# Optimization experiments

Hardware: AMD Instinct MI355X
Metric: run time of the kernel (lower is better)

## Reference

```python
import jax, jax.numpy as jnp
import numpy as np


def setup_inputs() -> dict:
    key = jax.random.key(0)
    k1, k2 = jax.random.split(key)
    N, C, H, W = 8, 3, 512, 1024
    img = jax.random.normal(k1, (N, C, H, W), dtype=jnp.float32)
    flo = jax.random.normal(k2, (N, 2, H, W), dtype=jnp.float32)
    return {"img": img, "flo": flo}


def _splat(img_nhwc, ix, iy, w, H, W):
    # img_nhwc: (N,H,W,C); ix,iy: int32 (N,H,W) absolute target coords; w: (N,H,W)
    N = img_nhwc.shape[0]
    C = img_nhwc.shape[-1]
    valid = (ix >= 0) & (ix < H) & (iy >= 0) & (iy < W)
    w = jnp.where(valid, w, 0.0)
    ixc = jnp.clip(ix, 0, H - 1)
    iyc = jnp.clip(iy, 0, W - 1)
    n_idx = jnp.arange(N, dtype=jnp.int32)[:, None, None]
    tid = (n_idx * H + ixc) * W + iyc            # (N,H,W) flat index into N*H*W
    tid = tid.reshape(-1)
    vals = (img_nhwc * w[..., None]).reshape(-1, C)
    imgw = jnp.zeros((N * H * W, C), dtype=img_nhwc.dtype).at[tid].add(vals)
    onew = jnp.zeros((N * H * W,), dtype=img_nhwc.dtype).at[tid].add(w.reshape(-1))
    imgw = imgw.reshape(N, H, W, C).transpose(0, 3, 1, 2)          # (N,C,H,W)
    onew = jnp.broadcast_to(onew.reshape(N, 1, H, W), (N, C, H, W))
    return imgw, onew


def _forward(img, flo):
    N, C, H, W = img.shape
    y = flo[:, 0]                                # (N,H,W) row offset
    x = flo[:, 1]                                # (N,H,W) col offset
    x1 = jnp.floor(x); x2 = x1 + 1.0
    y1 = jnp.floor(y); y2 = y1 + 1.0
    # gaussian splat weights
    dx1 = (x - x1) ** 2; dx2 = (x - x2) ** 2
    dy1 = (y - y1) ** 2; dy2 = (y - y2) ** 2
    w11 = jnp.exp(-(dx1 + dy1)); w12 = jnp.exp(-(dx1 + dy2))
    w21 = jnp.exp(-(dx2 + dy1)); w22 = jnp.exp(-(dx2 + dy2))
    # base grid + integer shift -> absolute target coords
    bx = jnp.arange(H, dtype=jnp.int32)[None, :, None]   # row index
    by = jnp.arange(W, dtype=jnp.int32)[None, None, :]   # col index
    img_nhwc = img.transpose(0, 2, 3, 1)
    out = []
    for sx, sy, w in ((x1, y1, w11), (x1, y2, w12), (x2, y1, w21), (x2, y2, w22)):
        ix = sx.astype(jnp.int32) + bx
        iy = sy.astype(jnp.int32) + by
        out.append(_splat(img_nhwc, ix, iy, w, H, W))
    imgw = out[0][0] + out[1][0] + out[2][0] + out[3][0]
    o = out[0][1] + out[1][1] + out[2][1] + out[3][1]
    return imgw, o


def reference(img, flo):
    return _forward(img, flo)
```

## Files before the change

kernel.cpp:

```cpp
#include <hip/hip_runtime.h>
#include <stdint.h>

constexpr int Nn = 8;
constexpr int Cc = 3;
constexpr int Hh = 512;
constexpr int Ww = 1024;
constexpr int HW = Hh * Ww;
constexpr int NCHW = Nn * Cc * HW;

constexpr int TH = 16;
constexpr int TW = 32;
constexpr int R  = 4;
constexpr int RH = TH + 2 * R;
constexpr int RW = TW + 2 * R;
constexpr int NPIX = RH * RW;
constexpr int ITERS = (NPIX + 255) / 256;
constexpr int TILE_PIX = TH * TW;
constexpr int AWP = TW + 1;
constexpr int NP  = (TH + 1) * AWP;
constexpr int OVF_SLOTS = 3;

typedef float fvec4 __attribute__((ext_vector_type(4)));
typedef __attribute__((address_space(3))) float lds_f;

__device__ __forceinline__ void ds_fadd4(lds_f* p, float a, float b, float c, float d) {
    asm volatile(
        "ds_add_f32 %0, %1\n\t"
        "ds_add_f32 %0, %2 offset:2048\n\t"
        "ds_add_f32 %0, %3 offset:4096\n\t"
        "ds_add_f32 %0, %4 offset:6144"
        :: "v"(p), "v"(a), "v"(b), "v"(c), "v"(d) : "memory");
}

__global__ __launch_bounds__(256, 3) void splat_tiled(
        const float* __restrict__ img,
        const float* __restrict__ flo,
        float* __restrict__ out) {
    __shared__ unsigned int s_tag[NP];
    __shared__ unsigned int s_ocnt[(NP + 3) / 4];
    __shared__ alignas(16) float s_pay[NP * 4];
    __shared__ alignas(16) float s_ovf[OVF_SLOTS * NP * 4];
    __shared__ float s_pl[4 * TILE_PIX];
    const int tid = threadIdx.x;
    for (int i = tid; i < NP; i += 256) s_tag[i] = 0u;
    for (int i = tid; i < (NP + 3) / 4; i += 256) s_ocnt[i] = 0u;
    {
        fvec4* a4 = (fvec4*)s_pl;
        fvec4 z = {0.f, 0.f, 0.f, 0.f};
        a4[tid] = z;
        a4[tid + 256] = z;
    }
    __syncthreads();

    const int lin = blockIdx.x + 32 * blockIdx.y + 1024 * blockIdx.z;
    const int n   = lin & 7;
    const int t   = lin >> 3;
    const int tw0 = (t & 31) * TW;
    const int th0 = (t >> 5) * TH;
    const float* __restrict__ floy = flo + (size_t)(n * 2 + 0) * HW;
    const float* __restrict__ flox = flo + (size_t)(n * 2 + 1) * HW;
    const float* __restrict__ imgn = img + (size_t)n * Cc * HW;

    float sy[ITERS], sx[ITERS], u0[ITERS], u1[ITERS], u2[ITERS];
    #pragma unroll
    for (int it = 0; it < ITERS; ++it) {
        int i  = tid + 256 * it;
        int ic = i < NPIX ? i : NPIX - 1;
        int rh = ic / RW;
        int rw = ic - rh * RW;
        int h  = th0 - R + rh;
        int w  = tw0 - R + rw;
        int hc = h < 0 ? 0 : (h > Hh - 1 ? Hh - 1 : h);
        int wc = w < 0 ? 0 : (w > Ww - 1 ? Ww - 1 : w);
        int hwc = hc * Ww + wc;
        sy[it] = floy[hwc];
        sx[it] = flox[hwc];
        u0[it] = imgn[hwc];
        u1[it] = imgn[HW + hwc];
        u2[it] = imgn[2 * HW + hwc];
    }

    int aA[ITERS];
    unsigned int tg[ITERS], fxy[ITERS];
    #pragma unroll
    for (int it = 0; it < ITERS; ++it) {
        int i  = tid + 256 * it;
        int rh = i / RW;
        int rw = i - rh * RW;
        int h  = th0 - R + rh;
        int w  = tw0 - R + rw;
        bool live = (i < NPIX) & (h >= 0) & (h < Hh) & (w >= 0) & (w < Ww);

        float y = sy[it], x = sx[it];
        float x1f = floorf(x), y1f = floorf(y);
        float fx = x - x1f, fy = y - y1f;
        int ox = (int)x1f, oy = (int)y1f;
        bool patchok = (ox >= -R) & (ox <= R - 1) & (oy >= -R) & (oy <= R - 1);
        int ah = ox + rh - R;
        int aw = oy + rw - R;
        bool rec = live & patchok & (ah >= -1) & (ah <= TH - 1)
                                  & (aw >= -1) & (aw <= TW - 1);
        int aIdx = (ah + 1) * AWP + (aw + 1);
        tg[it]  = 0x80000000u | ((unsigned)(ox + 4) << 24) | ((unsigned)(oy + 4) << 16);
        fxy[it] = (unsigned)(fx * 65535.0f + 0.5f)
                | ((unsigned)(fy * 65535.0f + 0.5f) << 16);
        aA[it]  = rec ? aIdx : -1;
        if (rec) s_tag[aIdx] = tg[it];
    }
    __syncthreads();

    #pragma unroll
    for (int it = 0; it < ITERS; ++it) {
        int a = aA[it];
        if (a >= 0) {
            if (s_tag[a] == tg[it]) {
                fvec4 e = {u0[it], u1[it], u2[it], __uint_as_float(fxy[it])};
                *(fvec4*)&s_pay[a * 4] = e;
            } else {
                unsigned sh  = 8u * (unsigned)(a & 3);
                unsigned old = atomicAdd(&s_ocnt[a >> 2], 1u << sh);
                unsigned idx = (old >> sh) & 0xFFu;
                if (idx < (unsigned)OVF_SLOTS) {
                    fvec4 e = {u0[it], u1[it], u2[it], __uint_as_float(fxy[it])};
                    *(fvec4*)&s_ovf[((int)idx * NP + a) * 4] = e;
                } else {
                    int ah = a / AWP - 1;
                    int aw = a - (ah + 1) * AWP - 1;
                    float fx = (float)(fxy[it] & 0xFFFFu) * (1.0f / 65535.0f);
                    float fy = (float)(fxy[it] >> 16) * (1.0f / 65535.0f);
                    #pragma unroll
                    for (int ca = 0; ca < 2; ++ca) {
                        #pragma unroll
                        for (int cb = 0; cb < 2; ++cb) {
                            int t_h = ah + ca, t_w = aw + cb;
                            if ((unsigned)t_h < (unsigned)TH && (unsigned)t_w < (unsigned)TW) {
                                float dx = fx - (float)ca, dy = fy - (float)cb;
                                float wt = __expf(-(dx * dx + dy * dy));
                                ds_fadd4((lds_f*)s_pl + (t_h * TW + t_w),
                                         u0[it] * wt, u1[it] * wt, u2[it] * wt, wt);
                            }
                        }
                    }
                }
            }
        }
    }
    __syncthreads();

    float* __restrict__ imgw  = out;
    float* __restrict__ o_out = out + NCHW;
    const size_t nb = (size_t)n * Cc * HW;
    const fvec4* pay4 = (const fvec4*)s_pay;
    const fvec4* ovf4 = (const fvec4*)s_ovf;
    #pragma unroll
    for (int itr = 0; itr < 2; ++itr) {
        int pix = tid + 256 * itr;
        int lh = pix >> 5, lw = pix & 31;
        float s0 = s_pl[pix];
        float s1 = s_pl[TILE_PIX + pix];
        float s2 = s_pl[2 * TILE_PIX + pix];
        float s3 = s_pl[3 * TILE_PIX + pix];
        #pragma unroll
        for (int a = 0; a < 2; ++a) {
            #pragma unroll
            for (int b = 0; b < 2; ++b) {
                int ai = (lh - a + 1) * AWP + (lw - b + 1);
                unsigned tgv = s_tag[ai];
                if (tgv & 0x80000000u) {
                    fvec4 e = pay4[ai];
                    unsigned p = __float_as_uint(e[3]);
                    float fx = (float)(p & 0xFFFFu) * (1.0f / 65535.0f);
                    float fy = (float)(p >> 16) * (1.0f / 65535.0f);
                    float dx = fx - (float)a, dy = fy - (float)b;
                    float wt = __expf(-(dx * dx + dy * dy));
                    s0 += e[0] * wt; s1 += e[1] * wt; s2 += e[2] * wt; s3 += wt;
                }
                unsigned k = (s_ocnt[ai >> 2] >> (8u * (unsigned)(ai & 3))) & 0xFFu;
                #pragma unroll
                for (int j = 0; j < OVF_SLOTS; ++j) {
                    if (j < (int)k) {
                        fvec4 e = ovf4[j * NP + ai];
                        unsigned p = __float_as_uint(e[3]);
                        float fx = (float)(p & 0xFFFFu) * (1.0f / 65535.0f);
                        float fy = (float)(p >> 16) * (1.0f / 65535.0f);
                        float dx = fx - (float)a, dy = fy - (float)b;
                        float wt = __expf(-(dx * dx + dy * dy));
                        s0 += e[0] * wt; s1 += e[1] * wt; s2 += e[2] * wt; s3 += wt;
                    }
                }
            }
        }
        size_t hw = (size_t)(th0 + lh) * Ww + (tw0 + lw);
        __builtin_nontemporal_store(s0, imgw + nb + hw);
        __builtin_nontemporal_store(s1, imgw + nb + HW + hw);
        __builtin_nontemporal_store(s2, imgw + nb + 2 * HW + hw);
        __builtin_nontemporal_store(s3, o_out + nb + hw);
        __builtin_nontemporal_store(s3, o_out + nb + HW + hw);
        __builtin_nontemporal_store(s3, o_out + nb + 2 * HW + hw);
    }
}

__global__ __launch_bounds__(256) void rescan_all(
        const float* __restrict__ img,
        const float* __restrict__ flo,
        float* __restrict__ out) {
    float* imgw  = out;
    float* o_out = out + NCHW;
    unsigned int j = blockIdx.x * blockDim.x + threadIdx.x;
    if (j >= (unsigned)(Nn * HW / 4)) return;
    int n   = j / (HW / 4);
    int q   = j - n * (HW / 4);
    int hw0 = q * 4;
    const fvec4 y4 = *(const fvec4*)&flo[(size_t)(n * 2 + 0) * HW + hw0];
    const fvec4 x4 = *(const fvec4*)&flo[(size_t)(n * 2 + 1) * HW + hw0];
    #pragma unroll
    for (int k = 0; k < 4; ++k) {
        float x = x4[k], y = y4[k];
        if (x >= -(float)R && x < (float)R && y >= -(float)R && y < (float)R) continue;
        int hw = hw0 + k;
        int h = hw >> 10;
        int w = hw & (Ww - 1);
        float x1f = floorf(x), y1f = floorf(y);
        float fx = x - x1f, fy = y - y1f;
        int bx = (int)x1f, by = (int)y1f;
        float i0 = img[(size_t)(n * Cc + 0) * HW + hw];
        float i1 = img[(size_t)(n * Cc + 1) * HW + hw];
        float i2 = img[(size_t)(n * Cc + 2) * HW + hw];
        const size_t nb = (size_t)n * Cc * HW;
        #pragma unroll
        for (int a = 0; a < 2; ++a) {
            #pragma unroll
            for (int b = 0; b < 2; ++b) {
                int ix = h + bx + a;
                int iy = w + by + b;
                if (ix < 0 || ix >= Hh || iy < 0 || iy >= Ww) continue;
                float dx = fx - (float)a, dy = fy - (float)b;
                float wt = __expf(-(dx * dx + dy * dy));
                int t = ix * Ww + iy;
                atomicAdd(&imgw[nb + t], i0 * wt);
                atomicAdd(&imgw[nb + HW + t], i1 * wt);
                atomicAdd(&imgw[nb + 2 * HW + t], i2 * wt);
                atomicAdd(&o_out[nb + t], wt);
                atomicAdd(&o_out[nb + HW + t], wt);
                atomicAdd(&o_out[nb + 2 * HW + t], wt);
            }
        }
    }
}

extern "C" void kernel_launch(void* const* d_in, const int* in_sizes, int n_in,
                              void* d_out, int out_size, void* d_ws, size_t ws_size,
                              hipStream_t stream) {
    const float* img = (const float*)d_in[0];
    const float* flo = (const float*)d_in[1];
    float* out = (float*)d_out;
    (void)d_ws; (void)ws_size;

    dim3 block(256);
    dim3 grid(32, 32, 8);
    splat_tiled<<<grid, block, 0, stream>>>(img, flo, out);
    rescan_all<<<(Nn * HW / 4 + 255) / 256, 256, 0, stream>>>(img, flo, out);
}
```

Baseline: 209.0 us.

## Compress splat payload to fp16 slots and resolve collisions in rounds

```diff
diff --git a/kernel.cpp b/kernel.cpp
--- a/kernel.cpp
+++ b/kernel.cpp
@@ -1,4 +1,5 @@
 #include <hip/hip_runtime.h>
+#include <hip/hip_fp16.h>
 #include <stdint.h>
 
 constexpr int Nn = 8;
@@ -18,9 +19,10 @@
 constexpr int TILE_PIX = TH * TW;
 constexpr int AWP = TW + 1;
 constexpr int NP  = (TH + 1) * AWP;
-constexpr int OVF_SLOTS = 3;
+constexpr int NSLOT = 3;
 
 typedef float fvec4 __attribute__((ext_vector_type(4)));
+typedef float fvec2 __attribute__((ext_vector_type(2)));
 typedef __attribute__((address_space(3))) float lds_f;
 
 __device__ __forceinline__ void ds_fadd4(lds_f* p, float a, float b, float c, float d) {
@@ -32,18 +34,17 @@
         :: "v"(p), "v"(a), "v"(b), "v"(c), "v"(d) : "memory");
 }
 
-__global__ __launch_bounds__(256, 3) void splat_tiled(
+__global__ __launch_bounds__(256, 5) void splat_tiled(
         const float* __restrict__ img,
         const float* __restrict__ flo,
         float* __restrict__ out) {
     __shared__ unsigned int s_tag[NP];
-    __shared__ unsigned int s_ocnt[(NP + 3) / 4];
-    __shared__ alignas(16) float s_pay[NP * 4];
-    __shared__ alignas(16) float s_ovf[OVF_SLOTS * NP * 4];
+    __shared__ unsigned int s_pay[NSLOT * NP * 3];
+    __shared__ unsigned int s_kcnt[(NP + 3) / 4 + 1];
     __shared__ float s_pl[4 * TILE_PIX];
     const int tid = threadIdx.x;
     for (int i = tid; i < NP; i += 256) s_tag[i] = 0u;
-    for (int i = tid; i < (NP + 3) / 4; i += 256) s_ocnt[i] = 0u;
+    for (int i = tid; i < (NP + 3) / 4 + 1; i += 256) s_kcnt[i] = 0u;
     {
         fvec4* a4 = (fvec4*)s_pl;
         fvec4 z = {0.f, 0.f, 0.f, 0.f};
@@ -81,7 +82,8 @@
     }
 
     int aA[ITERS];
-    unsigned int tg[ITERS], fxy[ITERS];
+    unsigned int tg[ITERS], q0[ITERS], q1[ITERS], q2[ITERS];
+    bool pend[ITERS];
     #pragma unroll
     for (int it = 0; it < ITERS; ++it) {
         int i  = tid + 256 * it;
@@ -101,102 +103,127 @@
         bool rec = live & patchok & (ah >= -1) & (ah <= TH - 1)
                                   & (aw >= -1) & (aw <= TW - 1);
         int aIdx = (ah + 1) * AWP + (aw + 1);
-        tg[it]  = 0x80000000u | ((unsigned)(ox + 4) << 24) | ((unsigned)(oy + 4) << 16);
-        fxy[it] = (unsigned)(fx * 65535.0f + 0.5f)
-                | ((unsigned)(fy * 65535.0f + 0.5f) << 16);
-        aA[it]  = rec ? aIdx : -1;
+        tg[it] = 0x80000000u | ((unsigned)(ox + R) << 3) | (unsigned)(oy + R);
+        unsigned h0 = __half_as_ushort(__float2half_rn(u0[it]));
+        unsigned h1 = __half_as_ushort(__float2half_rn(u1[it]));
+        unsigned h2 = __half_as_ushort(__float2half_rn(u2[it]));
+        unsigned fxq = (unsigned)(fx * 65535.0f + 0.5f);
+        unsigned fyq = (unsigned)(fy * 65535.0f + 0.5f);
+        q0[it] = h0 | (h1 << 16);
+        q1[it] = h2 | (fxq << 16);
+        q2[it] = fyq;
+        aA[it]  = aIdx;
+        pend[it] = rec;
         if (rec) s_tag[aIdx] = tg[it];
     }
     __syncthreads();
 
     #pragma unroll
-    for (int it = 0; it < ITERS; ++it) {
-        int a = aA[it];
-        if (a >= 0) {
-            if (s_tag[a] == tg[it]) {
-                fvec4 e = {u0[it], u1[it], u2[it], __uint_as_float(fxy[it])};
-                *(fvec4*)&s_pay[a * 4] = e;
-            } else {
-                unsigned sh  = 8u * (unsigned)(a & 3);
-                unsigned old = atomicAdd(&s_ocnt[a >> 2], 1u << sh);
-                unsigned idx = (old >> sh) & 0xFFu;
-                if (idx < (unsigned)OVF_SLOTS) {
-                    fvec4 e = {u0[it], u1[it], u2[it], __uint_as_float(fxy[it])};
-                    *(fvec4*)&s_ovf[((int)idx * NP + a) * 4] = e;
-                } else {
-                    int ah = a / AWP - 1;
-                    int aw = a - (ah + 1) * AWP - 1;
-                    float fx = (float)(fxy[it] & 0xFFFFu) * (1.0f / 65535.0f);
-                    float fy = (float)(fxy[it] >> 16) * (1.0f / 65535.0f);
+    for (int r = 0; r < NSLOT; ++r) {
+        #pragma unroll
+        for (int it = 0; it < ITERS; ++it) {
+            if (pend[it] && s_tag[aA[it]] == tg[it]) {
+                int base = aA[it] * 9 + r * 3;
+                s_pay[base]     = q0[it];
+                s_pay[base + 1] = q1[it];
+                s_pay[base + 2] = q2[it];
+                ((unsigned char*)s_kcnt)[aA[it]] = (unsigned char)(r + 1);
+                pend[it] = false;
+            } else if (r == NSLOT - 1 && pend[it]) {
+                int a = aA[it];
+                int arow = a / AWP;
+                int ah = arow - 1;
+                int aw = a - arow * AWP - 1;
+                float fx = (float)(q1[it] >> 16) * (1.0f / 65535.0f);
+                float fy = (float)(q2[it] & 0xFFFFu) * (1.0f / 65535.0f);
+                float i0 = __half2float(__ushort_as_half((unsigned short)(q0[it] & 0xFFFFu)));
+                float i1 = __half2float(__ushort_as_half((unsigned short)(q0[it] >> 16)));
+                float i2 = __half2float(__ushort_as_half((unsigned short)(q1[it] & 0xFFFFu)));
+                #pragma unroll
+                for (int ca = 0; ca < 2; ++ca) {
                     #pragma unroll
-                    for (int ca = 0; ca < 2; ++ca) {
-                        #pragma unroll
-                        for (int cb = 0; cb < 2; ++cb) {
-                            int t_h = ah + ca, t_w = aw + cb;
-                            if ((unsigned)t_h < (unsigned)TH && (unsigned)t_w < (unsigned)TW) {
-                                float dx = fx - (float)ca, dy = fy - (float)cb;
-                                float wt = __expf(-(dx * dx + dy * dy));
-                                ds_fadd4((lds_f*)s_pl + (t_h * TW + t_w),
-                                         u0[it] * wt, u1[it] * wt, u2[it] * wt, wt);
-                            }
+                    for (int cb = 0; cb < 2; ++cb) {
+                        int t_h = ah + ca, t_w = aw + cb;
+                        if ((unsigned)t_h < (unsigned)TH && (unsigned)t_w < (unsigned)TW) {
+                            float dx = fx - (float)ca, dy = fy - (float)cb;
+                            float wt = __expf(-(dx * dx + dy * dy));
+                            ds_fadd4((lds_f*)s_pl + (t_h * TW + t_w),
+                                     i0 * wt, i1 * wt, i2 * wt, wt);
                         }
                     }
                 }
             }
         }
-    }
-    __syncthreads();
+        __syncthreads();
+        if (r < NSLOT - 1) {
+            #pragma unroll
+            for (int it = 0; it < ITERS; ++it)
+                if (pend[it]) s_tag[aA[it]] = tg[it];
+            __syncthreads();
+        }
+    }
 
     float* __restrict__ imgw  = out;
     float* __restrict__ o_out = out + NCHW;
     const size_t nb = (size_t)n * Cc * HW;
-    const fvec4* pay4 = (const fvec4*)s_pay;
-    const fvec4* ovf4 = (const fvec4*)s_ovf;
-    #pragma unroll
-    for (int itr = 0; itr < 2; ++itr) {
-        int pix = tid + 256 * itr;
+    {
+        int pix = 2 * tid;
         int lh = pix >> 5, lw = pix & 31;
-        float s0 = s_pl[pix];
-        float s1 = s_pl[TILE_PIX + pix];
-        float s2 = s_pl[2 * TILE_PIX + pix];
-        float s3 = s_pl[3 * TILE_PIX + pix];
+        fvec2 p0 = *(const fvec2*)&s_pl[pix];
+        fvec2 p1 = *(const fvec2*)&s_pl[512 + pix];
+        fvec2 p2 = *(const fvec2*)&s_pl[1024 + pix];
+        fvec2 p3 = *(const fvec2*)&s_pl[1536 + pix];
+        float s0a = p0[0], s0b = p0[1];
+        float s1a = p1[0], s1b = p1[1];
+        float s2a = p2[0], s2b = p2[1];
+        float s3a = p3[0], s3b = p3[1];
         #pragma unroll
         for (int a = 0; a < 2; ++a) {
+            int arow = (lh - a + 1) * AWP + lw;
             #pragma unroll
-            for (int b = 0; b < 2; ++b) {
-                int ai = (lh - a + 1) * AWP + (lw - b + 1);
-                unsigned tgv = s_tag[ai];
-                if (tgv & 0x80000000u) {
-                    fvec4 e = pay4[ai];
-                    unsigned p = __float_as_uint(e[3]);
-                    float fx = (float)(p & 0xFFFFu) * (1.0f / 65535.0f);
-                    float fy = (float)(p >> 16) * (1.0f / 65535.0f);
-                    float dx = fx - (float)a, dy = fy - (float)b;
-                    float wt = __expf(-(dx * dx + dy * dy));
-                    s0 += e[0] * wt; s1 += e[1] * wt; s2 += e[2] * wt; s3 += wt;
-                }
-                unsigned k = (s_ocnt[ai >> 2] >> (8u * (unsigned)(ai & 3))) & 0xFFu;
+            for (int c = 0; c < 3; ++c) {
+                int ai = arow + c;
+                int k = ((const unsigned char*)s_kcnt)[ai];
                 #pragma unroll
-                for (int j = 0; j < OVF_SLOTS; ++j) {
-                    if (j < (int)k) {
-                        fvec4 e = ovf4[j * NP + ai];
-                        unsigned p = __float_as_uint(e[3]);
-                        float fx = (float)(p & 0xFFFFu) * (1.0f / 65535.0f);
-                        float fy = (float)(p >> 16) * (1.0f / 65535.0f);
-                        float dx = fx - (float)a, dy = fy - (float)b;
-                        float wt = __expf(-(dx * dx + dy * dy));
-                        s0 += e[0] * wt; s1 += e[1] * wt; s2 += e[2] * wt; s3 += wt;
+                for (int j = 0; j < NSLOT; ++j) {
+                    if (j < k) {
+                        int base = ai * 9 + j * 3;
+                        unsigned w0 = s_pay[base];
+                        unsigned w1 = s_pay[base + 1];
+                        unsigned w2 = s_pay[base + 2];
+                        float h0 = __half2float(__ushort_as_half((unsigned short)(w0 & 0xFFFFu)));
+                        float h1 = __half2float(__ushort_as_half((unsigned short)(w0 >> 16)));
+                        float h2 = __half2float(__ushort_as_half((unsigned short)(w1 & 0xFFFFu)));
+                        float fx = (float)(w1 >> 16) * (1.0f / 65535.0f);
+                        float fy = (float)(w2 & 0xFFFFu) * (1.0f / 65535.0f);
+                        float dx  = fx - (float)a;
+                        float dxx = dx * dx;
+                        if (c < 2) {
+                            float dy = fy - (float)(1 - c);
+                            float wt = __expf(-(dxx + dy * dy));
+                            s0a += h0 * wt; s1a += h1 * wt; s2a += h2 * wt; s3a += wt;
+                        }
+                        if (c >= 1) {
+                            float dy = fy - (float)(2 - c);
+                            float wt = __expf(-(dxx + dy * dy));
+                            s0b += h0 * wt; s1b += h1 * wt; s2b += h2 * wt; s3b += wt;
+                        }
                     }
                 }
             }
         }
         size_t hw = (size_t)(th0 + lh) * Ww + (tw0 + lw);
-        __builtin_nontemporal_store(s0, imgw + nb + hw);
-        __builtin_nontemporal_store(s1, imgw + nb + HW + hw);
-        __builtin_nontemporal_store(s2, imgw + nb + 2 * HW + hw);
-        __builtin_nontemporal_store(s3, o_out + nb + hw);
-        __builtin_nontemporal_store(s3, o_out + nb + HW + hw);
-        __builtin_nontemporal_store(s3, o_out + nb + 2 * HW + hw);
+        fvec2 v;
+        v[0] = s0a; v[1] = s0b;
+        __builtin_nontemporal_store(v, (fvec2*)(imgw + nb + hw));
+        v[0] = s1a; v[1] = s1b;
+        __builtin_nontemporal_store(v, (fvec2*)(imgw + nb + HW + hw));
+        v[0] = s2a; v[1] = s2b;
+        __builtin_nontemporal_store(v, (fvec2*)(imgw + nb + 2 * HW + hw));
+        v[0] = s3a; v[1] = s3b;
+        __builtin_nontemporal_store(v, (fvec2*)(o_out + nb + hw));
+        __builtin_nontemporal_store(v, (fvec2*)(o_out + nb + HW + hw));
+        __builtin_nontemporal_store(v, (fvec2*)(o_out + nb + 2 * HW + hw));
     }
 }
 
```

Result: faster. 191.1 us (-8.6%).
